# Performance work log

Hardware: AMD Instinct MI355X
Metric: run time of the kernel (lower is better)

## Reference

```python
import jax, jax.numpy as jnp
import numpy as np

N = 50000      # nodes
E = 800000     # edges (before self-loops)
DIN = 128      # input feature dim
DOUT = 128     # per-head output dim
H = 4          # heads (concat=False -> mean over heads)
SLOPE = 0.2    # PyG GATConv default negative_slope


def setup_inputs() -> dict:
    key = jax.random.key(0)
    k1, k2, k3, k4, k5 = jax.random.split(key, 5)
    x = jax.random.normal(k1, (N, DIN), dtype=jnp.float32)
    edge_index = jax.random.randint(k2, (2, E), 0, N)
    W = jax.random.normal(k3, (DIN, H * DOUT), dtype=jnp.float32) / np.sqrt(DIN).astype(np.float32)
    att_src = jax.random.normal(k4, (H, DOUT), dtype=jnp.float32) * 0.1
    att_dst = jax.random.normal(k5, (H, DOUT), dtype=jnp.float32) * 0.1
    return {"x": x, "edge_index": edge_index, "W": W, "att_src": att_src, "att_dst": att_dst}


def _gat(x, W, att_src, att_dst, src, dst):
    h = (x @ W).reshape(N, H, DOUT)                      # [N,H,C] shared lin for src/dst
    a_s = jnp.einsum('nhc,hc->nh', h, att_src)           # [N,H]
    a_d = jnp.einsum('nhc,hc->nh', h, att_dst)           # [N,H]
    logits = jax.nn.leaky_relu(a_s[src] + a_d[dst], SLOPE)   # [Etot,H]
    m = jax.ops.segment_max(logits, dst, num_segments=N)     # segment softmax (stable)
    e = jnp.exp(logits - m[dst])
    denom = jax.ops.segment_sum(e, dst, num_segments=N)
    alpha = e / (denom[dst] + 1e-16)                         # [Etot,H]
    out = jax.ops.segment_sum(alpha[:, :, None] * h[src], dst, num_segments=N)  # [N,H,C]
    return out.mean(axis=1)                                   # concat=False -> average heads


def reference(x, edge_index, W, att_src, att_dst):
    loop = jnp.arange(N, dtype=edge_index.dtype)          # add_self_loops=True (PyG default)
    src = jnp.concatenate([edge_index[0], loop])
    dst = jnp.concatenate([edge_index[1], loop])
    return _gat(x, W, att_src, att_dst, src, dst)
```

## Files before the change

### kernel.cpp

```cpp
#include <hip/hip_runtime.h>

#define NN 50000
#define EE 800000
#define ETOT (EE + NN)
#define MAXD 64
#define NBK 196
#define CAP 6144
#define P1B 128
#define CHP 6656

typedef _Float16 f16x8 __attribute__((ext_vector_type(8)));
typedef _Float16 f16x2 __attribute__((ext_vector_type(2)));
typedef float f32x4 __attribute__((ext_vector_type(4)));
typedef float f32x2 __attribute__((ext_vector_type(2)));
typedef unsigned int u32x4 __attribute__((ext_vector_type(4)));

__device__ __forceinline__ float lrelu(float v) { return v > 0.f ? v : 0.2f * v; }
__device__ __forceinline__ unsigned int pack2(float a, float b) {
  unsigned short lo = __builtin_bit_cast(unsigned short, (_Float16)a);
  unsigned short hi = __builtin_bit_cast(unsigned short, (_Float16)b);
  return (unsigned int)lo | ((unsigned int)hi << 16);
}

__global__ void k_prep(const float* __restrict__ W,
                       const float* __restrict__ att_s,
                       const float* __restrict__ att_d,
                       unsigned short* __restrict__ Bt,
                       float* __restrict__ WaS, float* __restrict__ WaD,
                       int* __restrict__ bcnt) {
  int gid = blockIdx.x * blockDim.x + threadIdx.x;
  if (gid < NBK) bcnt[gid] = 0;
  if (gid < 128 * 512) {
    int col = gid >> 9, k = gid & 511;
    float v = W[(k & 127) * 512 + (k >> 7) * 128 + col];
    _Float16 hv = (_Float16)v;
    Bt[col * 512 + k] = __builtin_bit_cast(unsigned short, hv);
  }
  if (gid < 512) {
    int k = gid >> 2, h = gid & 3;
    const float* wrow = W + k * 512 + h * 128;
    const float* as = att_s + h * 128;
    const float* ad = att_d + h * 128;
    float ss = 0.f, sd = 0.f;
    for (int c = 0; c < 128; ++c) { float w = wrow[c]; ss += w * as[c]; sd += w * ad[c]; }
    WaS[k * 4 + h] = ss;
    WaD[k * 4 + h] = sd;
  }
}

__global__ __launch_bounds__(256) void k_xcast_p1(const float* __restrict__ x,
                                                  const float* __restrict__ WaS,
                                                  const float* __restrict__ WaD,
                                                  const int* __restrict__ ei,
                                                  unsigned int* __restrict__ xh,
                                                  float* __restrict__ a_s,
                                                  float* __restrict__ a_d,
                                                  int* __restrict__ bcnt,
                                                  unsigned int* __restrict__ ebuf) {
  __shared__ unsigned long long D[128][33];
  __shared__ float4 wsl[128];
  __shared__ float4 wdl[128];
  __shared__ int cnt[NBK];
  __shared__ int gbase[NBK];
  int t = threadIdx.x;
  int nb = blockIdx.x * 128;
  if (t < 128) wsl[t] = ((const float4*)WaS)[t];
  else wdl[t - 128] = ((const float4*)WaD)[t - 128];
  for (int i = t; i < NBK; i += 256) cnt[i] = 0;

#pragma unroll
  for (int i = 0; i < 16; ++i) {
    int idx = t + i * 256;
    int n = idx >> 5, c4 = idx & 31;
    int gn = nb + n;
    float4 v = make_float4(0.f, 0.f, 0.f, 0.f);
    if (gn < NN) v = ((const float4*)x)[(size_t)gn * 32 + c4];
    unsigned int lo = pack2(v.x, v.y);
    unsigned int hi = pack2(v.z, v.w);
    if (gn < NN) ((uint2*)xh)[(size_t)gn * 32 + c4] = make_uint2(lo, hi);
    D[n][c4] = (unsigned long long)lo | ((unsigned long long)hi << 32);
  }
  __syncthreads();

  {
    int n = t >> 1, half = t & 1;
    float s0 = 0.f, s1 = 0.f, s2 = 0.f, s3 = 0.f;
    float d0 = 0.f, d1 = 0.f, d2 = 0.f, d3 = 0.f;
#pragma unroll
    for (int p = 0; p < 16; ++p) {
      int c4 = 2 * p + half;
      unsigned long long q = D[n][c4];
      f16x2 lo2 = __builtin_bit_cast(f16x2, (unsigned int)q);
      f16x2 hi2 = __builtin_bit_cast(f16x2, (unsigned int)(q >> 32));
      float f0 = (float)lo2[0], f1 = (float)lo2[1];
      float f2 = (float)hi2[0], f3 = (float)hi2[1];
      int c = c4 * 4;
      float4 w0 = wsl[c], w1 = wsl[c + 1], w2 = wsl[c + 2], w3 = wsl[c + 3];
      s0 += f0 * w0.x + f1 * w1.x + f2 * w2.x + f3 * w3.x;
      s1 += f0 * w0.y + f1 * w1.y + f2 * w2.y + f3 * w3.y;
      s2 += f0 * w0.z + f1 * w1.z + f2 * w2.z + f3 * w3.z;
      s3 += f0 * w0.w + f1 * w1.w + f2 * w2.w + f3 * w3.w;
      float4 v0 = wdl[c], v1 = wdl[c + 1], v2 = wdl[c + 2], v3 = wdl[c + 3];
      d0 += f0 * v0.x + f1 * v1.x + f2 * v2.x + f3 * v3.x;
      d1 += f0 * v0.y + f1 * v1.y + f2 * v2.y + f3 * v3.y;
      d2 += f0 * v0.z + f1 * v1.z + f2 * v2.z + f3 * v3.z;
      d3 += f0 * v0.w + f1 * v1.w + f2 * v2.w + f3 * v3.w;
    }
    s0 += __shfl_xor(s0, 1); s1 += __shfl_xor(s1, 1);
    s2 += __shfl_xor(s2, 1); s3 += __shfl_xor(s3, 1);
    d0 += __shfl_xor(d0, 1); d1 += __shfl_xor(d1, 1);
    d2 += __shfl_xor(d2, 1); d3 += __shfl_xor(d3, 1);
    int gn = nb + n;
    if (half == 0 && gn < NN) {
      *(float4*)(a_s + gn * 4) = make_float4(s0, s1, s2, s3);
      *(float4*)(a_d + gn * 4) = make_float4(d0, d1, d2, d3);
    }
  }

  if (blockIdx.x >= P1B) return;
  int e0 = blockIdx.x * CHP;
#pragma unroll
  for (int k = 0; k < CHP / 256; ++k) {
    int e = e0 + t + k * 256;
    if (e < ETOT) {
      int d = (e < EE) ? ei[EE + e] : (e - EE);
      atomicAdd(&cnt[d >> 8], 1);
    }
  }
  __syncthreads();
  for (int i = t; i < NBK; i += 256) {
    gbase[i] = (cnt[i] > 0) ? atomicAdd(&bcnt[i], cnt[i]) : 0;
    cnt[i] = 0;
  }
  __syncthreads();
#pragma unroll
  for (int k = 0; k < CHP / 256; ++k) {
    int e = e0 + t + k * 256;
    if (e < ETOT) {
      int s, d;
      if (e < EE) { s = ei[e]; d = ei[EE + e]; } else { s = d = e - EE; }
      int b = d >> 8;
      int idx = gbase[b] + atomicAdd(&cnt[b], 1);
      if (idx < CAP)
        ebuf[(size_t)b * CAP + idx] = (unsigned int)s | ((unsigned int)(d & 255) << 16);
    }
  }
}

__global__ __launch_bounds__(256) void k_p2(const unsigned int* __restrict__ ebuf,
                                            const int* __restrict__ bcnt,
                                            int* __restrict__ rs,
                                            unsigned short* __restrict__ perm16) {
  __shared__ int sb[256];
  __shared__ int loc[256];
  __shared__ int cnt[256];
  __shared__ unsigned short out16[CAP];
  __shared__ int basesh;
  int b = blockIdx.x, t = threadIdx.x;

  int v = (t < NBK) ? bcnt[t] : 0;
  sb[t] = v;
  __syncthreads();
  for (int off = 1; off < 256; off <<= 1) {
    int u = (t >= off) ? sb[t - off] : 0;
    __syncthreads();
    sb[t] += u;
    __syncthreads();
  }
  if (t == b) basesh = sb[t] - v;
  cnt[t] = 0;
  __syncthreads();

  int base = basesh;
  int m = min(bcnt[b], CAP);
  int d0 = b * 256;
  const unsigned int* rec = ebuf + (size_t)b * CAP;
  for (int i = t; i < m; i += 256) atomicAdd(&cnt[rec[i] >> 16], 1);
  __syncthreads();

  int c = cnt[t];
  sb[t] = c;
  __syncthreads();
  for (int off = 1; off < 256; off <<= 1) {
    int u = (t >= off) ? sb[t - off] : 0;
    __syncthreads();
    sb[t] += u;
    __syncthreads();
  }
  int ex = sb[t] - c;
  loc[t] = ex;
  int gi = d0 + t;
  if (gi < NN) rs[gi] = base + ex;
  if (b == NBK - 1 && t == 0) rs[NN] = base + m;
  cnt[t] = 0;
  __syncthreads();

  for (int i = t; i < m; i += 256) {
    unsigned int r = rec[i];
    int dl = r >> 16;
    int rk = atomicAdd(&cnt[dl], 1);
    out16[loc[dl] + rk] = (unsigned short)(r & 0xffffu);
  }
  __syncthreads();
  for (int i = t; i < m; i += 256) perm16[base + i] = out16[i];
}

__global__ __launch_bounds__(256) void k_aggz(const float* __restrict__ a_s,
                                              const float* __restrict__ a_d,
                                              const unsigned int* __restrict__ xh,
                                              const int* __restrict__ rs,
                                              const unsigned short* __restrict__ perm16,
                                              unsigned int* __restrict__ zbuf) {
  __shared__ unsigned int off_s[4][MAXD];
  __shared__ float4 w_s[4][MAXD];
  int wave = threadIdx.x >> 6, lane = threadIdx.x & 63;
  int n = blockIdx.x * 4 + wave;
  float4 ad = *(const float4*)(a_d + n * 4);
  int s = rs[n], e = rs[n + 1];
  int deg = e - s;
  bool fast = (deg <= MAXD);

  float t0 = 0.f, t1 = 0.f, t2 = 0.f, t3 = 0.f;
  if (fast) {
    if (lane < deg) {
      int sn = perm16[s + lane];
      off_s[wave][lane] = (unsigned int)sn * 256u;
      float4 as = *(const float4*)(a_s + sn * 4);
      float e0 = __expf(lrelu(as.x + ad.x));
      float e1 = __expf(lrelu(as.y + ad.y));
      float e2 = __expf(lrelu(as.z + ad.z));
      float e3 = __expf(lrelu(as.w + ad.w));
      w_s[wave][lane] = make_float4(e0, e1, e2, e3);
      t0 = e0; t1 = e1; t2 = e2; t3 = e3;
    }
  } else {
    for (int j = lane; j < deg; j += 64) {
      int sn = perm16[s + j];
      float4 as = *(const float4*)(a_s + sn * 4);
      t0 += __expf(lrelu(as.x + ad.x)); t1 += __expf(lrelu(as.y + ad.y));
      t2 += __expf(lrelu(as.z + ad.z)); t3 += __expf(lrelu(as.w + ad.w));
    }
  }
#pragma unroll
  for (int off = 32; off; off >>= 1) {
    t0 += __shfl_xor(t0, off); t1 += __shfl_xor(t1, off);
    t2 += __shfl_xor(t2, off); t3 += __shfl_xor(t3, off);
  }
  float sc0 = 0.25f / (t0 + 1e-16f), sc1 = 0.25f / (t1 + 1e-16f);
  float sc2 = 0.25f / (t2 + 1e-16f), sc3 = 0.25f / (t3 + 1e-16f);
  __builtin_amdgcn_wave_barrier();

  const char* xb = (const char*)xh;
  int lb = lane * 4;
  f32x2 za0 = {0.f, 0.f}, za1 = {0.f, 0.f}, za2 = {0.f, 0.f}, za3 = {0.f, 0.f};
  if (fast) {
    int j = 0;
    for (; j + 4 <= deg; j += 4) {
      unsigned int u[4];
#pragma unroll
      for (int k = 0; k < 4; ++k)
        u[k] = *(const unsigned int*)(xb + off_s[wave][j + k] + lb);
#pragma unroll
      for (int k = 0; k < 4; ++k) {
        float4 w = w_s[wave][j + k];
        f16x2 p = __builtin_bit_cast(f16x2, u[k]);
        f32x2 xv = {(float)p[0], (float)p[1]};
        za0 += w.x * xv; za1 += w.y * xv; za2 += w.z * xv; za3 += w.w * xv;
      }
    }
    for (; j < deg; ++j) {
      float4 w = w_s[wave][j];
      unsigned int u = *(const unsigned int*)(xb + off_s[wave][j] + lb);
      f16x2 p = __builtin_bit_cast(f16x2, u);
      f32x2 xv = {(float)p[0], (float)p[1]};
      za0 += w.x * xv; za1 += w.y * xv; za2 += w.z * xv; za3 += w.w * xv;
    }
  } else {
    for (int j = 0; j < deg; ++j) {
      int sn = perm16[s + j];
      float4 as = *(const float4*)(a_s + sn * 4);
      float w0 = __expf(lrelu(as.x + ad.x));
      float w1 = __expf(lrelu(as.y + ad.y));
      float w2 = __expf(lrelu(as.z + ad.z));
      float w3 = __expf(lrelu(as.w + ad.w));
      unsigned int u = xh[sn * 64 + lane];
      f16x2 p = __builtin_bit_cast(f16x2, u);
      f32x2 xv = {(float)p[0], (float)p[1]};
      za0 += w0 * xv; za1 += w1 * xv; za2 += w2 * xv; za3 += w3 * xv;
    }
  }

  zbuf[n * 256 + 0 * 64 + lane] = pack2(za0[0] * sc0, za0[1] * sc0);
  zbuf[n * 256 + 1 * 64 + lane] = pack2(za1[0] * sc1, za1[1] * sc1);
  zbuf[n * 256 + 2 * 64 + lane] = pack2(za2[0] * sc2, za2[1] * sc2);
  zbuf[n * 256 + 3 * 64 + lane] = pack2(za3[0] * sc3, za3[1] * sc3);
}

__global__ __launch_bounds__(256) void k_gemmz(const unsigned short* __restrict__ zbuf,
                                               const unsigned short* __restrict__ Bt,
                                               float* __restrict__ out) {
  __shared__ u32x4 Al[1024];
  __shared__ u32x4 Bl[2048];
  int m0 = blockIdx.x * 64;
  int wave = threadIdx.x >> 6, lane = threadIdx.x & 63;
  int wm = (wave >> 1) * 32, wn = (wave & 1) * 64;
  int lr = lane & 15, lk = lane >> 4;

  f32x4 acc[2][4];
#pragma unroll
  for (int mi = 0; mi < 2; ++mi)
#pragma unroll
    for (int ni = 0; ni < 4; ++ni) acc[mi][ni] = (f32x4){0.f, 0.f, 0.f, 0.f};

  for (int t = 0; t < 4; ++t) {
#pragma unroll
    for (int i = 0; i < 4; ++i) {
      int id = threadIdx.x + 256 * i;
      int row = id >> 4, kc = id & 15;
      int grow = m0 + row;
      u32x4 v = {0u, 0u, 0u, 0u};
      if (grow < NN) v = *(const u32x4*)((const char*)zbuf + grow * 1024 + t * 256 + kc * 16);
      Al[row * 16 + (kc ^ (row & 7))] = v;
    }
#pragma unroll
    for (int i = 0; i < 8; ++i) {
      int id = threadIdx.x + 256 * i;
      int col = id >> 4, kc = id & 15;
      u32x4 v = *(const u32x4*)((const char*)Bt + col * 1024 + t * 256 + kc * 16);
      Bl[col * 16 + (kc ^ (col & 7))] = v;
    }
    __syncthreads();
#pragma unroll
    for (int ks = 0; ks < 4; ++ks) {
      f16x8 af[2], bf[4];
#pragma unroll
      for (int mi = 0; mi < 2; ++mi) {
        int r = wm + mi * 16 + lr;
        af[mi] = __builtin_bit_cast(f16x8, Al[r * 16 + ((ks * 4 + lk) ^ (r & 7))]);
      }
#pragma unroll
      for (int ni = 0; ni < 4; ++ni) {
        int c = wn + ni * 16 + lr;
        bf[ni] = __builtin_bit_cast(f16x8, Bl[c * 16 + ((ks * 4 + lk) ^ (c & 7))]);
      }
#pragma unroll
      for (int mi = 0; mi < 2; ++mi)
#pragma unroll
        for (int ni = 0; ni < 4; ++ni)
          acc[mi][ni] = __builtin_amdgcn_mfma_f32_16x16x32_f16(af[mi], bf[ni], acc[mi][ni], 0, 0, 0);
    }
    __syncthreads();
  }

  int cr = lk * 4;
#pragma unroll
  for (int mi = 0; mi < 2; ++mi) {
#pragma unroll
    for (int j = 0; j < 4; ++j) {
      int row = m0 + wm + mi * 16 + cr + j;
      if (row < NN) {
#pragma unroll
        for (int ni = 0; ni < 4; ++ni) {
          int col = wn + ni * 16 + lr;
          out[row * 128 + col] = acc[mi][ni][j];
        }
      }
    }
  }
}

extern "C" void kernel_launch(void* const* d_in, const int* in_sizes, int n_in,
                              void* d_out, int out_size, void* d_ws, size_t ws_size,
                              hipStream_t stream) {
  const float* x = (const float*)d_in[0];
  const int* ei = (const int*)d_in[1];
  const float* W = (const float*)d_in[2];
  const float* att_s = (const float*)d_in[3];
  const float* att_d = (const float*)d_in[4];
  float* out = (float*)d_out;
  char* ws = (char*)d_ws;

  unsigned int* xh = (unsigned int*)(ws + 0);
  unsigned int* zbuf = (unsigned int*)(ws + 12800000);
  unsigned int* ebuf = (unsigned int*)(ws + 12800000);
  unsigned short* Bt = (unsigned short*)(ws + 64000000);
  float* WaS = (float*)(ws + 64131072);
  float* WaD = (float*)(ws + 64133120);
  float* a_s = (float*)(ws + 64135168);
  float* a_d = (float*)(ws + 64935168);
  int* rs = (int*)(ws + 65735168);
  int* bcnt = (int*)(ws + 65935360);
  unsigned short* perm16 = (unsigned short*)(ws + 65936384);

  k_prep<<<256, 256, 0, stream>>>(W, att_s, att_d, Bt, WaS, WaD, bcnt);
  k_xcast_p1<<<(NN + 127) / 128, 256, 0, stream>>>(x, WaS, WaD, ei, xh, a_s, a_d, bcnt, ebuf);
  k_p2<<<NBK, 256, 0, stream>>>(ebuf, bcnt, rs, perm16);
  k_aggz<<<NN / 4, 256, 0, stream>>>(a_s, a_d, xh, rs, perm16, zbuf);
  k_gemmz<<<(NN + 63) / 64, 256, 0, stream>>>((const unsigned short*)zbuf, Bt, out);
}
```

Baseline: 123.0 us.

## Spread edge binning across all blocks and drop LDS staging of x

Edge bucketing previously ran on only the first 128 blocks, with large chunks per block. It now runs on every node block with a smaller chunk size, so the binning load is spread evenly across the grid. The 33KB LDS tile holding the fp16 copy of x is removed. The per-node attention projections are now computed after binning, by re-reading fp32 x (likely still in cache) and multiplying against the shared weights. This cuts LDS use, which should raise occupancy, and slightly changes numerics because the projections now use fp32 x instead of the fp16-rounded values. The cost is an extra global read of x.

```diff
diff --git a/kernel.cpp b/kernel.cpp
--- a/kernel.cpp
+++ b/kernel.cpp
@@ -6,8 +6,7 @@
 #define MAXD 64
 #define NBK 196
 #define CAP 6144
-#define P1B 128
-#define CHP 6656
+#define CHX 2304
 
 typedef _Float16 f16x8 __attribute__((ext_vector_type(8)));
 typedef _Float16 f16x2 __attribute__((ext_vector_type(2)));
@@ -57,7 +56,6 @@
                                                   float* __restrict__ a_d,
                                                   int* __restrict__ bcnt,
                                                   unsigned int* __restrict__ ebuf) {
-  __shared__ unsigned long long D[128][33];
   __shared__ float4 wsl[128];
   __shared__ float4 wdl[128];
   __shared__ int cnt[NBK];
@@ -73,54 +71,17 @@
     int idx = t + i * 256;
     int n = idx >> 5, c4 = idx & 31;
     int gn = nb + n;
-    float4 v = make_float4(0.f, 0.f, 0.f, 0.f);
-    if (gn < NN) v = ((const float4*)x)[(size_t)gn * 32 + c4];
-    unsigned int lo = pack2(v.x, v.y);
-    unsigned int hi = pack2(v.z, v.w);
-    if (gn < NN) ((uint2*)xh)[(size_t)gn * 32 + c4] = make_uint2(lo, hi);
-    D[n][c4] = (unsigned long long)lo | ((unsigned long long)hi << 32);
-  }
-  __syncthreads();
-
-  {
-    int n = t >> 1, half = t & 1;
-    float s0 = 0.f, s1 = 0.f, s2 = 0.f, s3 = 0.f;
-    float d0 = 0.f, d1 = 0.f, d2 = 0.f, d3 = 0.f;
-#pragma unroll
-    for (int p = 0; p < 16; ++p) {
-      int c4 = 2 * p + half;
-      unsigned long long q = D[n][c4];
-      f16x2 lo2 = __builtin_bit_cast(f16x2, (unsigned int)q);
-      f16x2 hi2 = __builtin_bit_cast(f16x2, (unsigned int)(q >> 32));
-      float f0 = (float)lo2[0], f1 = (float)lo2[1];
-      float f2 = (float)hi2[0], f3 = (float)hi2[1];
-      int c = c4 * 4;
-      float4 w0 = wsl[c], w1 = wsl[c + 1], w2 = wsl[c + 2], w3 = wsl[c + 3];
-      s0 += f0 * w0.x + f1 * w1.x + f2 * w2.x + f3 * w3.x;
-      s1 += f0 * w0.y + f1 * w1.y + f2 * w2.y + f3 * w3.y;
-      s2 += f0 * w0.z + f1 * w1.z + f2 * w2.z + f3 * w3.z;
-      s3 += f0 * w0.w + f1 * w1.w + f2 * w2.w + f3 * w3.w;
-      float4 v0 = wdl[c], v1 = wdl[c + 1], v2 = wdl[c + 2], v3 = wdl[c + 3];
-      d0 += f0 * v0.x + f1 * v1.x + f2 * v2.x + f3 * v3.x;
-      d1 += f0 * v0.y + f1 * v1.y + f2 * v2.y + f3 * v3.y;
-      d2 += f0 * v0.z + f1 * v1.z + f2 * v2.z + f3 * v3.z;
-      d3 += f0 * v0.w + f1 * v1.w + f2 * v2.w + f3 * v3.w;
-    }
-    s0 += __shfl_xor(s0, 1); s1 += __shfl_xor(s1, 1);
-    s2 += __shfl_xor(s2, 1); s3 += __shfl_xor(s3, 1);
-    d0 += __shfl_xor(d0, 1); d1 += __shfl_xor(d1, 1);
-    d2 += __shfl_xor(d2, 1); d3 += __shfl_xor(d3, 1);
-    int gn = nb + n;
-    if (half == 0 && gn < NN) {
-      *(float4*)(a_s + gn * 4) = make_float4(s0, s1, s2, s3);
-      *(float4*)(a_d + gn * 4) = make_float4(d0, d1, d2, d3);
-    }
-  }
-
-  if (blockIdx.x >= P1B) return;
-  int e0 = blockIdx.x * CHP;
-#pragma unroll
-  for (int k = 0; k < CHP / 256; ++k) {
+    if (gn < NN) {
+      float4 v = ((const float4*)x)[(size_t)gn * 32 + c4];
+      ((uint2*)xh)[(size_t)gn * 32 + c4] =
+          make_uint2(pack2(v.x, v.y), pack2(v.z, v.w));
+    }
+  }
+  __syncthreads();
+
+  int e0 = blockIdx.x * CHX;
+#pragma unroll
+  for (int k = 0; k < CHX / 256; ++k) {
     int e = e0 + t + k * 256;
     if (e < ETOT) {
       int d = (e < EE) ? ei[EE + e] : (e - EE);
@@ -134,7 +95,7 @@
   }
   __syncthreads();
 #pragma unroll
-  for (int k = 0; k < CHP / 256; ++k) {
+  for (int k = 0; k < CHX / 256; ++k) {
     int e = e0 + t + k * 256;
     if (e < ETOT) {
       int s, d;
@@ -143,6 +104,47 @@
       int idx = gbase[b] + atomicAdd(&cnt[b], 1);
       if (idx < CAP)
         ebuf[(size_t)b * CAP + idx] = (unsigned int)s | ((unsigned int)(d & 255) << 16);
+    }
+  }
+
+  {
+    int n = t >> 1, half = t & 1;
+    int gn = nb + n;
+    if (gn < NN) {
+      const float4* xp = (const float4*)x + (size_t)gn * 32 + half;
+      float s0 = 0.f, s1 = 0.f, s2 = 0.f, s3 = 0.f;
+      float d0 = 0.f, d1 = 0.f, d2 = 0.f, d3 = 0.f;
+#pragma unroll
+      for (int p = 0; p < 16; p += 4) {
+        float4 v0 = xp[2 * p];
+        float4 v1 = xp[2 * (p + 1)];
+        float4 v2 = xp[2 * (p + 2)];
+        float4 v3 = xp[2 * (p + 3)];
+#define ACC(vv, pp)                                                        \
+        {                                                                  \
+          int c = 8 * (pp) + half * 4;                                     \
+          float4 w0 = wsl[c], w1 = wsl[c + 1], w2 = wsl[c + 2], w3 = wsl[c + 3]; \
+          s0 += vv.x * w0.x + vv.y * w1.x + vv.z * w2.x + vv.w * w3.x;     \
+          s1 += vv.x * w0.y + vv.y * w1.y + vv.z * w2.y + vv.w * w3.y;     \
+          s2 += vv.x * w0.z + vv.y * w1.z + vv.z * w2.z + vv.w * w3.z;     \
+          s3 += vv.x * w0.w + vv.y * w1.w + vv.z * w2.w + vv.w * w3.w;     \
+          float4 u0 = wdl[c], u1 = wdl[c + 1], u2 = wdl[c + 2], u3 = wdl[c + 3]; \
+          d0 += vv.x * u0.x + vv.y * u1.x + vv.z * u2.x + vv.w * u3.x;     \
+          d1 += vv.x * u0.y + vv.y * u1.y + vv.z * u2.y + vv.w * u3.y;     \
+          d2 += vv.x * u0.z + vv.y * u1.z + vv.z * u2.z + vv.w * u3.z;     \
+          d3 += vv.x * u0.w + vv.y * u1.w + vv.z * u2.w + vv.w * u3.w;     \
+        }
+        ACC(v0, p); ACC(v1, p + 1); ACC(v2, p + 2); ACC(v3, p + 3);
+#undef ACC
+      }
+      s0 += __shfl_xor(s0, 1); s1 += __shfl_xor(s1, 1);
+      s2 += __shfl_xor(s2, 1); s3 += __shfl_xor(s3, 1);
+      d0 += __shfl_xor(d0, 1); d1 += __shfl_xor(d1, 1);
+      d2 += __shfl_xor(d2, 1); d3 += __shfl_xor(d3, 1);
+      if (half == 0) {
+        *(float4*)(a_s + gn * 4) = make_float4(s0, s1, s2, s3);
+        *(float4*)(a_d + gn * 4) = make_float4(d0, d1, d2, d3);
+      }
     }
   }
 }
```

Measured after the change: 117.1 us. -4.8%, faster.
